# Optimization experiments

Hardware: AMD Instinct MI355X
Metric: run time of the kernel (lower is better)

The kernel has to match this reference:

```python
import jax, jax.numpy as jnp
import numpy as np

N = 4096      # n_nodes
IN = 256      # in_features
H = 4         # n_heads
F = 64        # out_features (per head)
SLOPE = 0.2   # leaky relu negative slope


def setup_inputs() -> dict:
    key = jax.random.key(0)
    k0, k1, k2, k3 = jax.random.split(key, 4)
    h = jax.random.normal(k0, (N, IN), dtype=jnp.float32)
    adj = jax.random.randint(k1, (N, N), 0, 2, dtype=jnp.int32)
    # ensure every node has at least one neighbor (self-loop) so softmax is defined
    adj = jnp.maximum(adj, jnp.eye(N, dtype=jnp.int32))
    # linear: in_features -> out_features * n_heads (xavier-ish scale)
    W = jax.random.normal(k2, (H * F, IN), dtype=jnp.float32) * np.float32(1.0 / np.sqrt(IN))
    b = jnp.zeros((H * F,), dtype=jnp.float32)
    # attn: Linear(2*F -> 1), weight row vector of size 2F plus scalar bias
    attn_w = jax.random.normal(k3, (2 * F,), dtype=jnp.float32) * np.float32(1.0 / np.sqrt(2 * F))
    attn_b = jnp.zeros((1,), dtype=jnp.float32)
    return {"h": h, "adj_mat": adj, "W": W, "b": b, "attn_w": attn_w, "attn_b": attn_b}


def reference(h, adj_mat, W, b, attn_w, attn_b):
    n = h.shape[0]
    # node projection: [N, H, F]
    g = (h @ W.T + b).reshape(n, H, F)
    # attn(concat(h_i, h_j)) = <a_src, g_i> + <a_dst, g_j> + bias  (decomposed, same math)
    src = jnp.einsum('nhf,f->nh', g, attn_w[:F])   # [N, H] contribution of node i
    dst = jnp.einsum('nhf,f->nh', g, attn_w[F:])   # [N, H] contribution of node j
    e = src[:, None, :] + dst[None, :, :] + attn_b[0]   # [N, N, H]
    e = jnp.where(e >= 0, e, SLOPE * e)                 # leaky relu
    e = jnp.where(adj_mat[:, :, None] != 0, e, -jnp.inf)  # mask non-edges
    a = jax.nn.softmax(e, axis=1)                       # softmax over neighbors j
    out = jnp.einsum('ijh,jhf->ihf', a, g)              # [N, H, F]
    return out.mean(axis=1)                             # average heads -> [N, F]
```

## Files before the change

kernel.cpp:

```cpp
#include <hip/hip_runtime.h>
#include <stdint.h>

constexpr int NODES = 4096;
constexpr int KIN   = 256;
constexpr int NHEAD = 4;
constexpr int NF    = 64;
constexpr int HFQ   = 256;
#define L2E 1.44269504088896340736f

typedef __attribute__((ext_vector_type(8))) short short8;
typedef __attribute__((ext_vector_type(4))) float floatx4;

static __device__ __forceinline__ unsigned short f2bf(float f) {
  return __builtin_bit_cast(unsigned short, (__bf16)f);
}

__global__ __launch_bounds__(256) void pack_prep_kernel(
    const int* __restrict__ adj, unsigned* __restrict__ bm,
    const float* __restrict__ hin, const float* __restrict__ Win,
    unsigned short* __restrict__ hB, unsigned short* __restrict__ WB) {
  int tid = threadIdx.x;
  if (blockIdx.x < 2048) {
    int wv = blockIdx.x * 4 + (tid >> 6);
    int lane = tid & 63;
    int jw = wv & 127;
    int it = wv >> 7;
    int i = it * 64 + lane;
    const int4* p = reinterpret_cast<const int4*>(adj + (size_t)i * NODES + jw * 32);
    unsigned m = 0;
#pragma unroll
    for (int q = 0; q < 8; ++q) {
      int4 a = p[q];
      m |= (a.x != 0 ? 1u : 0u) << (q * 4);
      m |= (a.y != 0 ? 1u : 0u) << (q * 4 + 1);
      m |= (a.z != 0 ? 1u : 0u) << (q * 4 + 2);
      m |= (a.w != 0 ? 1u : 0u) << (q * 4 + 3);
    }
    bm[(size_t)jw * NODES + i] = m;
  } else {
    int idx = (blockIdx.x - 2048) * 256 + tid;
    const int NH4 = (NODES * KIN) / 4;
    const int NW4 = (HFQ * KIN) / 4;
    if (idx < NH4) {
      float4 v = reinterpret_cast<const float4*>(hin)[idx];
      ushort4 o = { f2bf(v.x), f2bf(v.y), f2bf(v.z), f2bf(v.w) };
      reinterpret_cast<ushort4*>(hB)[idx] = o;
    } else if (idx < NH4 + NW4) {
      int j = idx - NH4;
      float4 v = reinterpret_cast<const float4*>(Win)[j];
      ushort4 o = { f2bf(v.x), f2bf(v.y), f2bf(v.z), f2bf(v.w) };
      reinterpret_cast<ushort4*>(WB)[j] = o;
    }
  }
}

__global__ __launch_bounds__(256) void proj_kernel(
    const unsigned short* __restrict__ hB, const unsigned short* __restrict__ WB,
    const float* __restrict__ bias, const float* __restrict__ attn_w,
    const float* __restrict__ attn_b,
    unsigned short* __restrict__ gT3, float2* __restrict__ srcP,
    unsigned* __restrict__ eP) {
  int h = threadIdx.x >> 6, lane = threadIdx.x & 63;
  int m0 = blockIdx.x * 16;
  int r = lane & 15, kg = lane >> 4;
  floatx4 acc[4] = {{0.f,0.f,0.f,0.f},{0.f,0.f,0.f,0.f},{0.f,0.f,0.f,0.f},{0.f,0.f,0.f,0.f}};
  const short8* Ap = reinterpret_cast<const short8*>(hB + (m0 + r) * KIN + kg * 8);
#pragma unroll
  for (int kb = 0; kb < 8; ++kb) {
    short8 a = Ap[kb * 4];
#pragma unroll
    for (int nt = 0; nt < 4; ++nt) {
      const short8 b = *reinterpret_cast<const short8*>(
          WB + (h * NF + nt * 16 + r) * KIN + kg * 8 + kb * 32);
      acc[nt] = __builtin_amdgcn_mfma_f32_16x16x32_bf16(a, b, acc[nt], 0, 0, 0);
    }
  }
  float ps[4] = {0.f,0.f,0.f,0.f}, pd[4] = {0.f,0.f,0.f,0.f};
#pragma unroll
  for (int nt = 0; nt < 4; ++nt) {
    int f = nt * 16 + r;
    float bv = bias[h * NF + f];
    float was = attn_w[f], wad = attn_w[64 + f];
#pragma unroll
    for (int q = 0; q < 4; ++q) {
      int row = m0 + kg * 4 + q;
      float v = acc[nt][q] + bv;
      int si = (row >> 5) * 8192 + h * 2048 + nt * 512 +
               (((row >> 3) & 3) * 16 + r) * 8 + (row & 7);
      gT3[si] = f2bf(v);
      ps[q] += v * was;
      pd[q] += v * wad;
    }
  }
#pragma unroll
  for (int m = 8; m >= 1; m >>= 1) {
#pragma unroll
    for (int q = 0; q < 4; ++q) {
      ps[q] += __shfl_xor(ps[q], m, 64);
      pd[q] += __shfl_xor(pd[q], m, 64);
    }
  }
  float ab = attn_b[0];
  if ((lane & 15) == 0) {
#pragma unroll
    for (int q = 0; q < 4; ++q) {
      int row = m0 + kg * 4 + q;
      float s = ps[q] + ab, d = pd[q];
      float2 sp;
      sp.x = exp2f(s * L2E);
      sp.y = exp2f(0.2f * s * L2E);
      srcP[row * NHEAD + h] = sp;
      float e1 = exp2f(d * L2E), e2 = exp2f(0.2f * d * L2E);
      eP[h * NODES + row] = ((unsigned)f2bf(e2) << 16) | (unsigned)f2bf(e1);
    }
  }
}

__global__ __launch_bounds__(256, 8) void attn_kernel(
    const unsigned* __restrict__ bm, const unsigned short* __restrict__ gT3,
    const float2* __restrict__ srcP, const unsigned* __restrict__ eP,
    float* __restrict__ pnum, float* __restrict__ pden, int JP) {
  int tid = threadIdx.x;
  int hh = tid >> 6, lane = tid & 63;
  int il = lane & 15, kg = lane >> 4;
  int part = blockIdx.x, itile = blockIdx.y;
  int jstart = part * JP;
  int i = itile * 16 + il;

  float2 sp = srcP[i * NHEAD + hh];
  float es1 = sp.x, es2 = sp.y;

  floatx4 acc0 = {0.f, 0.f, 0.f, 0.f};
  floatx4 acc1 = acc0, acc2 = acc0, acc3 = acc0, accd = acc0;

  short8 ones;
#pragma unroll
  for (int r = 0; r < 8; ++r) ones[r] = (short)0x3F80;

  int jt0 = jstart >> 5;
  const unsigned* bmp = bm + (size_t)jt0 * NODES + i;
  const unsigned* epp = eP + hh * NODES + jstart + kg * 8;
  const unsigned short* Atp = gT3 + (size_t)jt0 * 8192 + hh * 2048 + lane * 8;

  unsigned mwd = *bmp;
  uint4 ea = *reinterpret_cast<const uint4*>(epp);
  uint4 eb = *reinterpret_cast<const uint4*>(epp + 4);

  int nsteps = JP / 32;

#define STEP_BODY {                                                         \
    unsigned mb = (mwd >> (kg * 8)) & 0xFFu;                                \
    unsigned ev[8] = {ea.x, ea.y, ea.z, ea.w, eb.x, eb.y, eb.z, eb.w};      \
    short8 bfr;                                                             \
    _Pragma("unroll")                                                       \
    for (int r = 0; r < 8; ++r) {                                           \
      float e1f = __builtin_bit_cast(float, ev[r] << 16);                   \
      float e2f = __builtin_bit_cast(float, ev[r] & 0xFFFF0000u);           \
      float w = fmaxf(es1 * e1f, es2 * e2f);                                \
      w = (mb & (1u << r)) ? w : 0.f;                                       \
      bfr[r] = (short)f2bf(w);                                              \
    }                                                                       \
    const short8 a0 = *reinterpret_cast<const short8*>(Atp);                \
    const short8 a1 = *reinterpret_cast<const short8*>(Atp + 512);          \
    const short8 a2 = *reinterpret_cast<const short8*>(Atp + 1024);         \
    const short8 a3 = *reinterpret_cast<const short8*>(Atp + 1536);         \
    acc0 = __builtin_amdgcn_mfma_f32_16x16x32_bf16(a0, bfr, acc0, 0, 0, 0); \
    acc1 = __builtin_amdgcn_mfma_f32_16x16x32_bf16(a1, bfr, acc1, 0, 0, 0); \
    acc2 = __builtin_amdgcn_mfma_f32_16x16x32_bf16(a2, bfr, acc2, 0, 0, 0); \
    acc3 = __builtin_amdgcn_mfma_f32_16x16x32_bf16(a3, bfr, acc3, 0, 0, 0); \
    accd = __builtin_amdgcn_mfma_f32_16x16x32_bf16(ones, bfr, accd, 0, 0, 0);\
  }

  for (int stp = 0; stp < nsteps - 1; ++stp) {
    unsigned mwd_n = bmp[NODES];
    uint4 ea_n = *reinterpret_cast<const uint4*>(epp + 32);
    uint4 eb_n = *reinterpret_cast<const uint4*>(epp + 36);
    STEP_BODY;
    mwd = mwd_n; ea = ea_n; eb = eb_n;
    bmp += NODES; epp += 32; Atp += 8192;
  }
  STEP_BODY;
#undef STEP_BODY

  if (kg == 0)
    pden[(size_t)part * (NODES * NHEAD) + i * NHEAD + hh] = accd[0];

  float* pbase = pnum + (size_t)part * (NODES * HFQ) + (size_t)i * HFQ + hh * NF;
#pragma unroll
  for (int q = 0; q < 4; ++q) {
    int c = kg * 4 + q;
    pbase[c] = acc0[q];
    pbase[16 + c] = acc1[q];
    pbase[32 + c] = acc2[q];
    pbase[48 + c] = acc3[q];
  }
}

__global__ __launch_bounds__(256) void combine_kernel(
    const float* __restrict__ pnum, const float* __restrict__ pden,
    float* __restrict__ out, int NP) {
  int idx = blockIdx.x * 256 + threadIdx.x;
  int i = idx >> 6, f = idx & 63;
  float o = 0.f;
#pragma unroll
  for (int hh = 0; hh < NHEAD; ++hh) {
    float num = 0.f, den = 0.f;
    for (int p = 0; p < NP; ++p) {
      num += pnum[p * (NODES * HFQ) + i * HFQ + hh * NF + f];
      den += pden[p * (NODES * NHEAD) + i * NHEAD + hh];
    }
    o += num / den;
  }
  out[idx] = 0.25f * o;
}

extern "C" void kernel_launch(void* const* d_in, const int* in_sizes, int n_in,
                              void* d_out, int out_size, void* d_ws, size_t ws_size,
                              hipStream_t stream) {
  const float* hin = (const float*)d_in[0];
  const int* adj   = (const int*)d_in[1];
  const float* W   = (const float*)d_in[2];
  const float* b   = (const float*)d_in[3];
  const float* aw  = (const float*)d_in[4];
  const float* ab  = (const float*)d_in[5];
  float* out = (float*)d_out;
  char* ws = (char*)d_ws;

  unsigned short* hB  = (unsigned short*)(ws + 0x000000);
  unsigned short* WB  = (unsigned short*)(ws + 0x200000);
  unsigned short* gT3 = (unsigned short*)(ws + 0x400000);
  float2* srcP        = (float2*)(ws + 0x600000);
  unsigned* eP        = (unsigned*)(ws + 0x620000);
  unsigned* bm        = (unsigned*)(ws + 0x640000);
  float* pden         = (float*)(ws + 0x840000);
  float* pnum         = (float*)(ws + 0x900000);
  const size_t base = 0x900000;

  int NP = 2;
  if (ws_size >= base + 8ull * NODES * HFQ * 4) NP = 8;
  else if (ws_size >= base + 4ull * NODES * HFQ * 4) NP = 4;
  int JP = NODES / NP;

  pack_prep_kernel<<<2048 + 1088, 256, 0, stream>>>(adj, bm, hin, W, hB, WB);
  proj_kernel<<<256, 256, 0, stream>>>(hB, WB, b, aw, ab, gT3, srcP, eP);
  attn_kernel<<<dim3(NP, 256), 256, 0, stream>>>(bm, gT3, srcP, eP, pnum, pden, JP);
  combine_kernel<<<1024, 256, 0, stream>>>(pnum, pden, out, NP);
}
```

Before: 71.20 us.

## Precompute softmax denominators, fold head-mean into weights, shrink partial outputs

Adds a kernel that computes each node's per-head softmax denominator up front and folds 1/den and the 0.25 head-average into the source scale factors. The attention kernel drops its denominator MFMA, sums the four heads in shared memory, and writes partial outputs of size [N,64] instead of [N,256], so the combine kernel becomes a plain sum. The projection kernel is split across four times as many blocks, and the attention loop now prefetches its gT3 operands one step ahead. The cost is an extra pass over the bitmask and eP arrays, more register pressure (occupancy hint lowered from 8 to 6), and a denominator now accumulated in fp32 from bf16 values rather than the rounded bf16 weights used in the numerator.

```diff
diff --git a/kernel.cpp b/kernel.cpp
--- a/kernel.cpp
+++ b/kernel.cpp
@@ -60,66 +60,89 @@
     const float* __restrict__ attn_b,
     unsigned short* __restrict__ gT3, float2* __restrict__ srcP,
     unsigned* __restrict__ eP) {
-  int h = threadIdx.x >> 6, lane = threadIdx.x & 63;
-  int m0 = blockIdx.x * 16;
+  __shared__ float2 sred[4][16];
+  int nt = threadIdx.x >> 6, lane = threadIdx.x & 63;
+  int mt = blockIdx.x >> 2, h = blockIdx.x & 3;
+  int m0 = mt * 16;
   int r = lane & 15, kg = lane >> 4;
-  floatx4 acc[4] = {{0.f,0.f,0.f,0.f},{0.f,0.f,0.f,0.f},{0.f,0.f,0.f,0.f},{0.f,0.f,0.f,0.f}};
+  int col = h * NF + nt * 16 + r;
+  floatx4 acc = {0.f, 0.f, 0.f, 0.f};
   const short8* Ap = reinterpret_cast<const short8*>(hB + (m0 + r) * KIN + kg * 8);
-#pragma unroll
-  for (int kb = 0; kb < 8; ++kb) {
-    short8 a = Ap[kb * 4];
-#pragma unroll
-    for (int nt = 0; nt < 4; ++nt) {
-      const short8 b = *reinterpret_cast<const short8*>(
-          WB + (h * NF + nt * 16 + r) * KIN + kg * 8 + kb * 32);
-      acc[nt] = __builtin_amdgcn_mfma_f32_16x16x32_bf16(a, b, acc[nt], 0, 0, 0);
-    }
-  }
-  float ps[4] = {0.f,0.f,0.f,0.f}, pd[4] = {0.f,0.f,0.f,0.f};
-#pragma unroll
-  for (int nt = 0; nt < 4; ++nt) {
-    int f = nt * 16 + r;
-    float bv = bias[h * NF + f];
-    float was = attn_w[f], wad = attn_w[64 + f];
-#pragma unroll
-    for (int q = 0; q < 4; ++q) {
-      int row = m0 + kg * 4 + q;
-      float v = acc[nt][q] + bv;
-      int si = (row >> 5) * 8192 + h * 2048 + nt * 512 +
-               (((row >> 3) & 3) * 16 + r) * 8 + (row & 7);
-      gT3[si] = f2bf(v);
-      ps[q] += v * was;
-      pd[q] += v * wad;
-    }
-  }
-#pragma unroll
-  for (int m = 8; m >= 1; m >>= 1) {
+  const short8* Bp = reinterpret_cast<const short8*>(WB + col * KIN + kg * 8);
+#pragma unroll
+  for (int kb = 0; kb < 8; ++kb)
+    acc = __builtin_amdgcn_mfma_f32_16x16x32_bf16(Ap[kb * 4], Bp[kb * 4], acc, 0, 0, 0);
+  float bv = bias[col];
+  float was = attn_w[nt * 16 + r], wad = attn_w[64 + nt * 16 + r];
+  float ps[4], pd[4];
+#pragma unroll
+  for (int q = 0; q < 4; ++q) {
+    int row = m0 + kg * 4 + q;
+    float v = acc[q] + bv;
+    int si = (row >> 5) * 8192 + h * 2048 + nt * 512 +
+             (((row >> 3) & 3) * 16 + r) * 8 + (row & 7);
+    gT3[si] = f2bf(v);
+    ps[q] = v * was;
+    pd[q] = v * wad;
+  }
+#pragma unroll
+  for (int m = 8; m >= 1; m >>= 1)
 #pragma unroll
     for (int q = 0; q < 4; ++q) {
       ps[q] += __shfl_xor(ps[q], m, 64);
       pd[q] += __shfl_xor(pd[q], m, 64);
     }
-  }
-  float ab = attn_b[0];
-  if ((lane & 15) == 0) {
-#pragma unroll
-    for (int q = 0; q < 4; ++q) {
-      int row = m0 + kg * 4 + q;
-      float s = ps[q] + ab, d = pd[q];
-      float2 sp;
-      sp.x = exp2f(s * L2E);
-      sp.y = exp2f(0.2f * s * L2E);
-      srcP[row * NHEAD + h] = sp;
-      float e1 = exp2f(d * L2E), e2 = exp2f(0.2f * d * L2E);
-      eP[h * NODES + row] = ((unsigned)f2bf(e2) << 16) | (unsigned)f2bf(e1);
-    }
-  }
-}
-
-__global__ __launch_bounds__(256, 8) void attn_kernel(
+  if ((lane & 15) == 0)
+#pragma unroll
+    for (int q = 0; q < 4; ++q)
+      sred[nt][kg * 4 + q] = float2{ps[q], pd[q]};
+  __syncthreads();
+  if (threadIdx.x < 16) {
+    int row = threadIdx.x;
+    float s = sred[0][row].x + sred[1][row].x + sred[2][row].x + sred[3][row].x + attn_b[0];
+    float d = sred[0][row].y + sred[1][row].y + sred[2][row].y + sred[3][row].y;
+    float2 sp;
+    sp.x = exp2f(s * L2E);
+    sp.y = exp2f(0.2f * s * L2E);
+    srcP[(m0 + row) * NHEAD + h] = sp;
+    float e1 = exp2f(d * L2E), e2 = exp2f(0.2f * d * L2E);
+    eP[h * NODES + m0 + row] = ((unsigned)f2bf(e2) << 16) | (unsigned)f2bf(e1);
+  }
+}
+
+__global__ __launch_bounds__(256) void denscale_kernel(
+    const unsigned* __restrict__ bm, const unsigned* __restrict__ eP,
+    const float2* __restrict__ srcP, float2* __restrict__ srcP2) {
+  int wv = blockIdx.x * 4 + (threadIdx.x >> 6);
+  int lane = threadIdx.x & 63;
+  int h = wv & 3, i = wv >> 2;
+  float2 sp = srcP[i * NHEAD + h];
+  float es1 = sp.x, es2 = sp.y;
+  float den = 0.f;
+  const unsigned* ep = eP + h * NODES + lane;
+  const unsigned* bp = bm + i;
+  int sub = lane >> 5, bit = lane & 31;
+  for (int k = 0; k < 64; ++k) {
+    unsigned ev = ep[k * 64];
+    unsigned word = bp[(size_t)(k * 2 + sub) * NODES];
+    float e1f = __builtin_bit_cast(float, ev << 16);
+    float e2f = __builtin_bit_cast(float, ev & 0xFFFF0000u);
+    float w = fmaxf(es1 * e1f, es2 * e2f);
+    den += ((word >> bit) & 1u) ? w : 0.f;
+  }
+#pragma unroll
+  for (int m = 32; m >= 1; m >>= 1) den += __shfl_xor(den, m, 64);
+  if (lane == 0) {
+    float sc = 0.25f / den;
+    srcP2[i * NHEAD + h] = float2{es1 * sc, es2 * sc};
+  }
+}
+
+__global__ __launch_bounds__(256, 6) void attn_kernel(
     const unsigned* __restrict__ bm, const unsigned short* __restrict__ gT3,
-    const float2* __restrict__ srcP, const unsigned* __restrict__ eP,
-    float* __restrict__ pnum, float* __restrict__ pden, int JP) {
+    const float2* __restrict__ srcP2, const unsigned* __restrict__ eP,
+    float* __restrict__ pnum, int JP) {
+  __shared__ float red[4][16][68];
   int tid = threadIdx.x;
   int hh = tid >> 6, lane = tid & 63;
   int il = lane & 15, kg = lane >> 4;
@@ -127,15 +150,11 @@
   int jstart = part * JP;
   int i = itile * 16 + il;
 
-  float2 sp = srcP[i * NHEAD + hh];
+  float2 sp = srcP2[i * NHEAD + hh];
   float es1 = sp.x, es2 = sp.y;
 
   floatx4 acc0 = {0.f, 0.f, 0.f, 0.f};
-  floatx4 acc1 = acc0, acc2 = acc0, acc3 = acc0, accd = acc0;
-
-  short8 ones;
-#pragma unroll
-  for (int r = 0; r < 8; ++r) ones[r] = (short)0x3F80;
+  floatx4 acc1 = acc0, acc2 = acc0, acc3 = acc0;
 
   int jt0 = jstart >> 5;
   const unsigned* bmp = bm + (size_t)jt0 * NODES + i;
@@ -145,6 +164,10 @@
   unsigned mwd = *bmp;
   uint4 ea = *reinterpret_cast<const uint4*>(epp);
   uint4 eb = *reinterpret_cast<const uint4*>(epp + 4);
+  short8 a0 = *reinterpret_cast<const short8*>(Atp);
+  short8 a1 = *reinterpret_cast<const short8*>(Atp + 512);
+  short8 a2 = *reinterpret_cast<const short8*>(Atp + 1024);
+  short8 a3 = *reinterpret_cast<const short8*>(Atp + 1536);
 
   int nsteps = JP / 32;
 
@@ -160,58 +183,59 @@
       w = (mb & (1u << r)) ? w : 0.f;                                       \
       bfr[r] = (short)f2bf(w);                                              \
     }                                                                       \
-    const short8 a0 = *reinterpret_cast<const short8*>(Atp);                \
-    const short8 a1 = *reinterpret_cast<const short8*>(Atp + 512);          \
-    const short8 a2 = *reinterpret_cast<const short8*>(Atp + 1024);         \
-    const short8 a3 = *reinterpret_cast<const short8*>(Atp + 1536);         \
     acc0 = __builtin_amdgcn_mfma_f32_16x16x32_bf16(a0, bfr, acc0, 0, 0, 0); \
     acc1 = __builtin_amdgcn_mfma_f32_16x16x32_bf16(a1, bfr, acc1, 0, 0, 0); \
     acc2 = __builtin_amdgcn_mfma_f32_16x16x32_bf16(a2, bfr, acc2, 0, 0, 0); \
     acc3 = __builtin_amdgcn_mfma_f32_16x16x32_bf16(a3, bfr, acc3, 0, 0, 0); \
-    accd = __builtin_amdgcn_mfma_f32_16x16x32_bf16(ones, bfr, accd, 0, 0, 0);\
   }
 
   for (int stp = 0; stp < nsteps - 1; ++stp) {
-    unsigned mwd_n = bmp[NODES];
-    uint4 ea_n = *reinterpret_cast<const uint4*>(epp + 32);
-    uint4 eb_n = *reinterpret_cast<const uint4*>(epp + 36);
+    bmp += NODES; epp += 32; Atp += 8192;
+    unsigned mwd_n = *bmp;
+    uint4 ea_n = *reinterpret_cast<const uint4*>(epp);
+    uint4 eb_n = *reinterpret_cast<const uint4*>(epp + 4);
+    short8 a0n = *reinterpret_cast<const short8*>(Atp);
+    short8 a1n = *reinterpret_cast<const short8*>(Atp + 512);
+    short8 a2n = *reinterpret_cast<const short8*>(Atp + 1024);
+    short8 a3n = *reinterpret_cast<const short8*>(Atp + 1536);
     STEP_BODY;
     mwd = mwd_n; ea = ea_n; eb = eb_n;
-    bmp += NODES; epp += 32; Atp += 8192;
+    a0 = a0n; a1 = a1n; a2 = a2n; a3 = a3n;
   }
   STEP_BODY;
 #undef STEP_BODY
 
-  if (kg == 0)
-    pden[(size_t)part * (NODES * NHEAD) + i * NHEAD + hh] = accd[0];
-
-  float* pbase = pnum + (size_t)part * (NODES * HFQ) + (size_t)i * HFQ + hh * NF;
 #pragma unroll
   for (int q = 0; q < 4; ++q) {
-    int c = kg * 4 + q;
-    pbase[c] = acc0[q];
-    pbase[16 + c] = acc1[q];
-    pbase[32 + c] = acc2[q];
-    pbase[48 + c] = acc3[q];
-  }
+    red[hh][il][ 0 + kg * 4 + q] = acc0[q];
+    red[hh][il][16 + kg * 4 + q] = acc1[q];
+    red[hh][il][32 + kg * 4 + q] = acc2[q];
+    red[hh][il][48 + kg * 4 + q] = acc3[q];
+  }
+  __syncthreads();
+  int il2 = tid >> 4, cb = tid & 15;
+  const float4 v0 = *reinterpret_cast<const float4*>(&red[0][il2][cb * 4]);
+  const float4 v1 = *reinterpret_cast<const float4*>(&red[1][il2][cb * 4]);
+  const float4 v2 = *reinterpret_cast<const float4*>(&red[2][il2][cb * 4]);
+  const float4 v3 = *reinterpret_cast<const float4*>(&red[3][il2][cb * 4]);
+  float4 s;
+  s.x = v0.x + v1.x + v2.x + v3.x;
+  s.y = v0.y + v1.y + v2.y + v3.y;
+  s.z = v0.z + v1.z + v2.z + v3.z;
+  s.w = v0.w + v1.w + v2.w + v3.w;
+  *reinterpret_cast<float4*>(pnum + (size_t)part * (NODES * NF) +
+                             itile * 1024 + il2 * 64 + cb * 4) = s;
 }
 
 __global__ __launch_bounds__(256) void combine_kernel(
-    const float* __restrict__ pnum, const float* __restrict__ pden,
-    float* __restrict__ out, int NP) {
+    const float4* __restrict__ pnum, float4* __restrict__ out, int NP) {
   int idx = blockIdx.x * 256 + threadIdx.x;
-  int i = idx >> 6, f = idx & 63;
-  float o = 0.f;
-#pragma unroll
-  for (int hh = 0; hh < NHEAD; ++hh) {
-    float num = 0.f, den = 0.f;
-    for (int p = 0; p < NP; ++p) {
-      num += pnum[p * (NODES * HFQ) + i * HFQ + hh * NF + f];
-      den += pden[p * (NODES * NHEAD) + i * NHEAD + hh];
-    }
-    o += num / den;
-  }
-  out[idx] = 0.25f * o;
+  float4 s = pnum[idx];
+  for (int p = 1; p < NP; ++p) {
+    float4 v = pnum[p * (NODES * NF / 4) + idx];
+    s.x += v.x; s.y += v.y; s.z += v.z; s.w += v.w;
+  }
+  out[idx] = s;
 }
 
 extern "C" void kernel_launch(void* const* d_in, const int* in_sizes, int n_in,
@@ -228,21 +252,22 @@
 
   unsigned short* hB  = (unsigned short*)(ws + 0x000000);
   unsigned short* WB  = (unsigned short*)(ws + 0x200000);
+  float2* srcP        = (float2*)(ws + 0x220000);
+  float2* srcP2       = (float2*)(ws + 0x240000);
+  unsigned* eP        = (unsigned*)(ws + 0x260000);
   unsigned short* gT3 = (unsigned short*)(ws + 0x400000);
-  float2* srcP        = (float2*)(ws + 0x600000);
-  unsigned* eP        = (unsigned*)(ws + 0x620000);
-  unsigned* bm        = (unsigned*)(ws + 0x640000);
-  float* pden         = (float*)(ws + 0x840000);
-  float* pnum         = (float*)(ws + 0x900000);
-  const size_t base = 0x900000;
+  unsigned* bm        = (unsigned*)(ws + 0x600000);
+  float* pnum         = (float*)(ws + 0x800000);
+  const size_t base = 0x800000;
 
   int NP = 2;
-  if (ws_size >= base + 8ull * NODES * HFQ * 4) NP = 8;
-  else if (ws_size >= base + 4ull * NODES * HFQ * 4) NP = 4;
+  if (ws_size >= base + 8ull * NODES * NF * 4) NP = 8;
+  else if (ws_size >= base + 4ull * NODES * NF * 4) NP = 4;
   int JP = NODES / NP;
 
   pack_prep_kernel<<<2048 + 1088, 256, 0, stream>>>(adj, bm, hin, W, hB, WB);
-  proj_kernel<<<256, 256, 0, stream>>>(hB, WB, b, aw, ab, gT3, srcP, eP);
-  attn_kernel<<<dim3(NP, 256), 256, 0, stream>>>(bm, gT3, srcP, eP, pnum, pden, JP);
-  combine_kernel<<<1024, 256, 0, stream>>>(pnum, pden, out, NP);
-}
+  proj_kernel<<<1024, 256, 0, stream>>>(hB, WB, b, aw, ab, gT3, srcP, eP);
+  denscale_kernel<<<4096, 256, 0, stream>>>(bm, eP, srcP, srcP2);
+  attn_kernel<<<dim3(NP, 256), 256, 0, stream>>>(bm, gT3, srcP2, eP, pnum, JP);
+  combine_kernel<<<256, 256, 0, stream>>>((const float4*)pnum, (float4*)out, NP);
+}
```

Measured after the change: 80.03 us. 12.4% more time.

## Fuse bf16 conversion and projection GEMM into the adjacency-pack kernel

Applied to the files above, without the earlier changes.

Removes the separate proj kernel and the bf16 staging buffers for h and W. The projection now runs as extra blocks of the adjacency bit-packing kernel and converts fp32 inputs to bf16 in registers just before each MFMA. Work is split across 1024 blocks, one per (16-row tile, head) pair, and the per-head partial attention dot products are reduced through shared memory. This saves one kernel launch and a full round trip of bf16 h/W through memory, but each W tile is now reloaded as fp32 by more blocks.

```diff
diff --git a/kernel.cpp b/kernel.cpp
--- a/kernel.cpp
+++ b/kernel.cpp
@@ -15,10 +15,14 @@
   return __builtin_bit_cast(unsigned short, (__bf16)f);
 }
 
-__global__ __launch_bounds__(256) void pack_prep_kernel(
+__global__ __launch_bounds__(256) void prep_kernel(
     const int* __restrict__ adj, unsigned* __restrict__ bm,
     const float* __restrict__ hin, const float* __restrict__ Win,
-    unsigned short* __restrict__ hB, unsigned short* __restrict__ WB) {
+    const float* __restrict__ bias, const float* __restrict__ attn_w,
+    const float* __restrict__ attn_b,
+    unsigned short* __restrict__ gT3, float2* __restrict__ srcP,
+    unsigned* __restrict__ eP) {
+  __shared__ float2 sred[4][16];
   int tid = threadIdx.x;
   if (blockIdx.x < 2048) {
     int wv = blockIdx.x * 4 + (tid >> 6);
@@ -37,82 +41,69 @@
       m |= (a.w != 0 ? 1u : 0u) << (q * 4 + 3);
     }
     bm[(size_t)jw * NODES + i] = m;
-  } else {
-    int idx = (blockIdx.x - 2048) * 256 + tid;
-    const int NH4 = (NODES * KIN) / 4;
-    const int NW4 = (HFQ * KIN) / 4;
-    if (idx < NH4) {
-      float4 v = reinterpret_cast<const float4*>(hin)[idx];
-      ushort4 o = { f2bf(v.x), f2bf(v.y), f2bf(v.z), f2bf(v.w) };
-      reinterpret_cast<ushort4*>(hB)[idx] = o;
-    } else if (idx < NH4 + NW4) {
-      int j = idx - NH4;
-      float4 v = reinterpret_cast<const float4*>(Win)[j];
-      ushort4 o = { f2bf(v.x), f2bf(v.y), f2bf(v.z), f2bf(v.w) };
-      reinterpret_cast<ushort4*>(WB)[j] = o;
-    }
-  }
-}
-
-__global__ __launch_bounds__(256) void proj_kernel(
-    const unsigned short* __restrict__ hB, const unsigned short* __restrict__ WB,
-    const float* __restrict__ bias, const float* __restrict__ attn_w,
-    const float* __restrict__ attn_b,
-    unsigned short* __restrict__ gT3, float2* __restrict__ srcP,
-    unsigned* __restrict__ eP) {
-  int h = threadIdx.x >> 6, lane = threadIdx.x & 63;
-  int m0 = blockIdx.x * 16;
+    return;
+  }
+  int bid = blockIdx.x - 2048;
+  int nt = tid >> 6, lane = tid & 63;
+  int mt = bid >> 2, h = bid & 3;
+  int m0 = mt * 16;
   int r = lane & 15, kg = lane >> 4;
-  floatx4 acc[4] = {{0.f,0.f,0.f,0.f},{0.f,0.f,0.f,0.f},{0.f,0.f,0.f,0.f},{0.f,0.f,0.f,0.f}};
-  const short8* Ap = reinterpret_cast<const short8*>(hB + (m0 + r) * KIN + kg * 8);
+  int col = h * NF + nt * 16 + r;
+  floatx4 acc = {0.f, 0.f, 0.f, 0.f};
+  const float* Af = hin + (m0 + r) * KIN + kg * 8;
+  const float* Bf = Win + col * KIN + kg * 8;
 #pragma unroll
   for (int kb = 0; kb < 8; ++kb) {
-    short8 a = Ap[kb * 4];
-#pragma unroll
-    for (int nt = 0; nt < 4; ++nt) {
-      const short8 b = *reinterpret_cast<const short8*>(
-          WB + (h * NF + nt * 16 + r) * KIN + kg * 8 + kb * 32);
-      acc[nt] = __builtin_amdgcn_mfma_f32_16x16x32_bf16(a, b, acc[nt], 0, 0, 0);
-    }
-  }
-  float ps[4] = {0.f,0.f,0.f,0.f}, pd[4] = {0.f,0.f,0.f,0.f};
-#pragma unroll
-  for (int nt = 0; nt < 4; ++nt) {
-    int f = nt * 16 + r;
-    float bv = bias[h * NF + f];
-    float was = attn_w[f], wad = attn_w[64 + f];
-#pragma unroll
-    for (int q = 0; q < 4; ++q) {
-      int row = m0 + kg * 4 + q;
-      float v = acc[nt][q] + bv;
-      int si = (row >> 5) * 8192 + h * 2048 + nt * 512 +
-               (((row >> 3) & 3) * 16 + r) * 8 + (row & 7);
-      gT3[si] = f2bf(v);
-      ps[q] += v * was;
-      pd[q] += v * wad;
-    }
-  }
-#pragma unroll
-  for (int m = 8; m >= 1; m >>= 1) {
+    float4 fa0 = *reinterpret_cast<const float4*>(Af + kb * 32);
+    float4 fa1 = *reinterpret_cast<const float4*>(Af + kb * 32 + 4);
+    float4 fb0 = *reinterpret_cast<const float4*>(Bf + kb * 32);
+    float4 fb1 = *reinterpret_cast<const float4*>(Bf + kb * 32 + 4);
+    short8 a, b;
+    a[0] = (short)f2bf(fa0.x); a[1] = (short)f2bf(fa0.y);
+    a[2] = (short)f2bf(fa0.z); a[3] = (short)f2bf(fa0.w);
+    a[4] = (short)f2bf(fa1.x); a[5] = (short)f2bf(fa1.y);
+    a[6] = (short)f2bf(fa1.z); a[7] = (short)f2bf(fa1.w);
+    b[0] = (short)f2bf(fb0.x); b[1] = (short)f2bf(fb0.y);
+    b[2] = (short)f2bf(fb0.z); b[3] = (short)f2bf(fb0.w);
+    b[4] = (short)f2bf(fb1.x); b[5] = (short)f2bf(fb1.y);
+    b[6] = (short)f2bf(fb1.z); b[7] = (short)f2bf(fb1.w);
+    acc = __builtin_amdgcn_mfma_f32_16x16x32_bf16(a, b, acc, 0, 0, 0);
+  }
+  float bv = bias[col];
+  float was = attn_w[nt * 16 + r], wad = attn_w[64 + nt * 16 + r];
+  float ps[4], pd[4];
+#pragma unroll
+  for (int q = 0; q < 4; ++q) {
+    int row = m0 + kg * 4 + q;
+    float v = acc[q] + bv;
+    int si = (row >> 5) * 8192 + h * 2048 + nt * 512 +
+             (((row >> 3) & 3) * 16 + r) * 8 + (row & 7);
+    gT3[si] = f2bf(v);
+    ps[q] = v * was;
+    pd[q] = v * wad;
+  }
+#pragma unroll
+  for (int m = 8; m >= 1; m >>= 1)
 #pragma unroll
     for (int q = 0; q < 4; ++q) {
       ps[q] += __shfl_xor(ps[q], m, 64);
       pd[q] += __shfl_xor(pd[q], m, 64);
     }
-  }
-  float ab = attn_b[0];
-  if ((lane & 15) == 0) {
-#pragma unroll
-    for (int q = 0; q < 4; ++q) {
-      int row = m0 + kg * 4 + q;
-      float s = ps[q] + ab, d = pd[q];
-      float2 sp;
-      sp.x = exp2f(s * L2E);
-      sp.y = exp2f(0.2f * s * L2E);
-      srcP[row * NHEAD + h] = sp;
-      float e1 = exp2f(d * L2E), e2 = exp2f(0.2f * d * L2E);
-      eP[h * NODES + row] = ((unsigned)f2bf(e2) << 16) | (unsigned)f2bf(e1);
-    }
+  if ((lane & 15) == 0)
+#pragma unroll
+    for (int q = 0; q < 4; ++q)
+      sred[nt][kg * 4 + q] = float2{ps[q], pd[q]};
+  __syncthreads();
+  if (tid < 16) {
+    int row = tid;
+    float s = sred[0][row].x + sred[1][row].x + sred[2][row].x + sred[3][row].x + attn_b[0];
+    float d = sred[0][row].y + sred[1][row].y + sred[2][row].y + sred[3][row].y;
+    float2 sp;
+    sp.x = exp2f(s * L2E);
+    sp.y = exp2f(0.2f * s * L2E);
+    srcP[(m0 + row) * NHEAD + h] = sp;
+    float e1 = exp2f(d * L2E), e2 = exp2f(0.2f * d * L2E);
+    eP[h * NODES + m0 + row] = ((unsigned)f2bf(e2) << 16) | (unsigned)f2bf(e1);
   }
 }
 
@@ -226,23 +217,20 @@
   float* out = (float*)d_out;
   char* ws = (char*)d_ws;
 
-  unsigned short* hB  = (unsigned short*)(ws + 0x000000);
-  unsigned short* WB  = (unsigned short*)(ws + 0x200000);
-  unsigned short* gT3 = (unsigned short*)(ws + 0x400000);
-  float2* srcP        = (float2*)(ws + 0x600000);
-  unsigned* eP        = (unsigned*)(ws + 0x620000);
-  unsigned* bm        = (unsigned*)(ws + 0x640000);
-  float* pden         = (float*)(ws + 0x840000);
-  float* pnum         = (float*)(ws + 0x900000);
-  const size_t base = 0x900000;
+  unsigned short* gT3 = (unsigned short*)(ws + 0x000000);
+  float2* srcP        = (float2*)(ws + 0x200000);
+  unsigned* eP        = (unsigned*)(ws + 0x220000);
+  unsigned* bm        = (unsigned*)(ws + 0x240000);
+  float* pden         = (float*)(ws + 0x440000);
+  float* pnum         = (float*)(ws + 0x500000);
+  const size_t base = 0x500000;
 
   int NP = 2;
   if (ws_size >= base + 8ull * NODES * HFQ * 4) NP = 8;
   else if (ws_size >= base + 4ull * NODES * HFQ * 4) NP = 4;
   int JP = NODES / NP;
 
-  pack_prep_kernel<<<2048 + 1088, 256, 0, stream>>>(adj, bm, hin, W, hB, WB);
-  proj_kernel<<<256, 256, 0, stream>>>(hB, WB, b, aw, ab, gT3, srcP, eP);
+  prep_kernel<<<3072, 256, 0, stream>>>(adj, bm, hin, W, b, aw, ab, gT3, srcP, eP);
   attn_kernel<<<dim3(NP, 256), 256, 0, stream>>>(bm, gT3, srcP, eP, pnum, pden, JP);
   combine_kernel<<<1024, 256, 0, stream>>>(pnum, pden, out, NP);
 }
```

Result: slower. 78.74 us (+10.6%).
